# Optimization experiments

Measured on AMD Instinct MI355X. Metric: run time of the kernel, lower is better.

The kernel has to match this reference:

```python
import jax, jax.numpy as jnp
import numpy as np

SOBEL_X = jnp.array([[1., 0., -1.], [2., 0., -2.], [1., 0., -1.]], dtype=jnp.float32).reshape(1, 1, 3, 3)
SOBEL_Y = jnp.array([[1., 2., 1.], [0., 0., 0.], [-1., -2., -1.]], dtype=jnp.float32).reshape(1, 1, 3, 3)
EPS = 1e-3


def _sobel(img, kern):
    # img: [N, 1, H, W]; 3x3 conv, zero padding 1 (torch Conv2d padding=1)
    return jax.lax.conv_general_dilated(
        img, kern, window_strides=(1, 1), padding='SAME',
        dimension_numbers=('NCHW', 'OIHW', 'NCHW'))


def _compute_flow(frames):
    # frames: [B, T, 3, H, W] -> flow: [B, T-1, 2, H, W]
    B, T, C, H, W = frames.shape
    gray = (0.2989 * frames[:, :, 0] + 0.587 * frames[:, :, 1]
            + 0.114 * frames[:, :, 2])  # [B, T, H, W]
    I1 = gray[:, :-1].reshape(B * (T - 1), 1, H, W)
    I2 = gray[:, 1:].reshape(B * (T - 1), 1, H, W)
    Ix = _sobel(I1, SOBEL_X)
    Iy = _sobel(I1, SOBEL_Y)
    It = I2 - I1
    denom = Ix * Ix + Iy * Iy + EPS
    u = -Ix * It / denom
    v = -Iy * It / denom
    return jnp.concatenate([u, v], axis=1).reshape(B, T - 1, 2, H, W)


def setup_inputs() -> dict:
    key = jax.random.key(0)
    k1, k2 = jax.random.split(key)
    shape = (8, 8, 3, 256, 256)  # [B, T, C, H, W]
    pred = jax.random.uniform(k1, shape, dtype=jnp.float32)
    gt = jax.random.uniform(k2, shape, dtype=jnp.float32)
    return {"pred": pred, "gt": gt}


def reference(pred, gt):
    pred_flow = _compute_flow(pred)  # [B, T-1, 2, H, W]
    gt_flow = _compute_flow(gt)
    # motion magnitude: mean abs frame diff over channels, broadcast over 2 flow channels
    motion_mag = jnp.abs(gt[:, 1:] - gt[:, :-1]).mean(axis=2, keepdims=True)  # [B, T-1, 1, H, W]
    flow_loss = (jnp.abs(pred_flow - gt_flow) * motion_mag).mean()
    return flow_loss
```

## Files before the change

kernel.cpp:

```cpp
#include <hip/hip_runtime.h>

#define BB 8
#define TT 8
#define NPAIR (TT - 1)
#define HH 256
#define WW 256
#define FRAME_PIX (HH * WW)
#define RROWS 4
#define NSTRIP (HH / RROWS)
#define NITEM (BB * NPAIR * NSTRIP)
#define NBLK (NITEM / 4)
#define EPS 1e-3f
#define INV_N (1.0f / (float)((size_t)BB * NPAIR * 2 * HH * WW))

__device__ __forceinline__ float4 ld4(const float* __restrict__ p) {
    return *reinterpret_cast<const float4*>(p);
}
__device__ __forceinline__ float4 gray4(const float4 r, const float4 g, const float4 b) {
    float4 o;
    o.x = 0.2989f * r.x + 0.587f * g.x + 0.114f * b.x;
    o.y = 0.2989f * r.y + 0.587f * g.y + 0.114f * b.y;
    o.z = 0.2989f * r.z + 0.587f * g.z + 0.114f * b.z;
    o.w = 0.2989f * r.w + 0.587f * g.w + 0.114f * b.w;
    return o;
}

struct GRow { float l, a, b, c, d, r; };

__device__ __forceinline__ GRow mk_grow(const float4 g, const int lane) {
    GRow o;
    o.a = g.x; o.b = g.y; o.c = g.z; o.d = g.w;
    const float lw = __shfl_up(g.w, 1, 64);
    const float rx = __shfl_down(g.x, 1, 64);
    o.l = (lane == 0) ? 0.f : lw;
    o.r = (lane == 63) ? 0.f : rx;
    return o;
}

__device__ __forceinline__ void ld3(const float* __restrict__ base, const int y,
                                    const int X, float4& c0, float4& c1, float4& c2) {
    if ((unsigned)y < (unsigned)HH) {
        const float* q = base + (size_t)y * WW + X;
        c0 = ld4(q); c1 = ld4(q + FRAME_PIX); c2 = ld4(q + 2 * FRAME_PIX);
    } else {
        c0 = make_float4(0.f, 0.f, 0.f, 0.f); c1 = c0; c2 = c0;
    }
}

#define FLOWJ_P(T, M, Bt, f0, f1, f2, g2v, uj, vj)                              \
    {                                                                           \
        const float Ix = ((T).f0 - (T).f2) + 2.0f * ((M).f0 - (M).f2)           \
                       + ((Bt).f0 - (Bt).f2);                                   \
        const float Iy = ((T).f0 + 2.0f * (T).f1 + (T).f2)                      \
                       - ((Bt).f0 + 2.0f * (Bt).f1 + (Bt).f2);                  \
        const float It = (g2v) - (M).f1;                                        \
        const float inv = 1.0f / (Ix * Ix + Iy * Iy + EPS);                     \
        uj = -(Ix * It) * inv;                                                  \
        vj = -(Iy * It) * inv;                                                  \
    }

#define FLOWJ_G(T, M, Bt, f0, f1, f2, g2v, uj, vj, mmv)                         \
    {                                                                           \
        const float Ix = ((T).f0 - (T).f2) + 2.0f * ((M).f0 - (M).f2)           \
                       + ((Bt).f0 - (Bt).f2);                                   \
        const float Iy = ((T).f0 + 2.0f * (T).f1 + (T).f2)                      \
                       - ((Bt).f0 + 2.0f * (Bt).f1 + (Bt).f2);                  \
        const float It = (g2v) - (M).f1;                                        \
        const float inv = 1.0f / (Ix * Ix + Iy * Iy + EPS);                     \
        s += (fabsf((uj) + (Ix * It) * inv) + fabsf((vj) + (Iy * It) * inv))    \
             * (mmv);                                                           \
    }

#define STEP(ROWY)                                                              \
    {                                                                           \
        float4 pb0, pb1, pb2, gb0, gb1, gb2, pc0, pc1, pc2, gc0, gc1, gc2;      \
        ld3(p1, (ROWY) + 1, X, pb0, pb1, pb2);                                  \
        ld3(g1, (ROWY) + 1, X, gb0, gb1, gb2);                                  \
        ld3(p2, (ROWY), X, pc0, pc1, pc2);                                      \
        ld3(g2, (ROWY), X, gc0, gc1, gc2);                                      \
        const float mm0 = (fabsf(gc0.x - k0.x) + fabsf(gc1.x - k1.x)            \
                         + fabsf(gc2.x - k2.x)) * (1.f / 3.f);                  \
        const float mm1 = (fabsf(gc0.y - k0.y) + fabsf(gc1.y - k1.y)            \
                         + fabsf(gc2.y - k2.y)) * (1.f / 3.f);                  \
        const float mm2 = (fabsf(gc0.z - k0.z) + fabsf(gc1.z - k1.z)            \
                         + fabsf(gc2.z - k2.z)) * (1.f / 3.f);                  \
        const float mm3 = (fabsf(gc0.w - k0.w) + fabsf(gc1.w - k1.w)            \
                         + fabsf(gc2.w - k2.w)) * (1.f / 3.f);                  \
        const float4 gp2c = gray4(pc0, pc1, pc2);                               \
        const float4 gg2c = gray4(gc0, gc1, gc2);                               \
        const GRow pB = mk_grow(gray4(pb0, pb1, pb2), lane);                    \
        const GRow gB = mk_grow(gray4(gb0, gb1, gb2), lane);                    \
        k0 = gb0; k1 = gb1; k2 = gb2;                                           \
        float u0, u1, u2, u3, v0, v1, v2, v3;                                   \
        FLOWJ_P(pT, pM, pB, l, a, b, gp2c.x, u0, v0)                            \
        FLOWJ_P(pT, pM, pB, a, b, c, gp2c.y, u1, v1)                            \
        FLOWJ_P(pT, pM, pB, b, c, d, gp2c.z, u2, v2)                            \
        FLOWJ_P(pT, pM, pB, c, d, r, gp2c.w, u3, v3)                            \
        FLOWJ_G(gT, gM, gB, l, a, b, gg2c.x, u0, v0, mm0)                       \
        FLOWJ_G(gT, gM, gB, a, b, c, gg2c.y, u1, v1, mm1)                       \
        FLOWJ_G(gT, gM, gB, b, c, d, gg2c.z, u2, v2, mm2)                       \
        FLOWJ_G(gT, gM, gB, c, d, r, gg2c.w, u3, v3, mm3)                       \
        pT = pM; pM = pB;                                                       \
        gT = gM; gM = gB;                                                       \
    }

__global__ __launch_bounds__(256, 2) void flow_loss_kernel(
    const float* __restrict__ pred, const float* __restrict__ gt,
    float* __restrict__ partial)
{
    const int tid   = threadIdx.x;
    const int lane  = tid & 63;
    const int item  = blockIdx.x * 4 + (tid >> 6);
    const int strip = item & (NSTRIP - 1);
    const int pbt   = item >> 6;
    const int b     = pbt / NPAIR;
    const int t     = pbt - b * NPAIR;

    const size_t fs = (size_t)3 * FRAME_PIX;
    const float* p1 = pred + ((size_t)b * TT + t) * fs;
    const float* g1 = gt   + ((size_t)b * TT + t) * fs;
    const float* p2 = p1 + fs;
    const float* g2 = g1 + fs;

    const int X  = lane * 4;
    const int y0 = strip * RROWS;

    GRow pT, pM, gT, gM;
    float4 k0, k1, k2;

    {
        float4 a0, a1, a2, c0, c1, c2;
        ld3(p1, y0 - 1, X, a0, a1, a2);
        ld3(g1, y0 - 1, X, c0, c1, c2);
        pT = mk_grow(gray4(a0, a1, a2), lane);
        gT = mk_grow(gray4(c0, c1, c2), lane);
        ld3(p1, y0, X, a0, a1, a2);
        ld3(g1, y0, X, k0, k1, k2);
        pM = mk_grow(gray4(a0, a1, a2), lane);
        gM = mk_grow(gray4(k0, k1, k2), lane);
    }

    float s = 0.f;
    STEP(y0)
    STEP(y0 + 1)
    STEP(y0 + 2)
    STEP(y0 + 3)

    #pragma unroll
    for (int off = 32; off > 0; off >>= 1) s += __shfl_down(s, off, 64);
    if (lane == 0) partial[item] = s;
}

__global__ __launch_bounds__(896) void reduce_kernel(
    const float* __restrict__ partial, float* __restrict__ out)
{
    const float4 v = ld4(partial + threadIdx.x * 4);
    float s = (v.x + v.y) + (v.z + v.w);
    #pragma unroll
    for (int off = 32; off > 0; off >>= 1) s += __shfl_down(s, off, 64);

    __shared__ float wsum[14];
    if ((threadIdx.x & 63) == 0) wsum[threadIdx.x >> 6] = s;
    __syncthreads();
    if (threadIdx.x == 0) {
        float tot = 0.f;
        #pragma unroll
        for (int i = 0; i < 14; ++i) tot += wsum[i];
        out[0] = tot * INV_N;
    }
}

extern "C" void kernel_launch(void* const* d_in, const int* in_sizes, int n_in,
                              void* d_out, int out_size, void* d_ws, size_t ws_size,
                              hipStream_t stream) {
    const float* pred = (const float*)d_in[0];
    const float* gt   = (const float*)d_in[1];
    float* partial    = (float*)d_ws;
    float* out        = (float*)d_out;

    flow_loss_kernel<<<dim3(NBLK), dim3(256), 0, stream>>>(pred, gt, partial);
    reduce_kernel<<<1, 896, 0, stream>>>(partial, out);
}
```

Before: 124.1 us.

## Software-prefetch next frame-1 row and shrink blocks to two waves

Each step now issues the loads for the frame-1 row two ahead (y+2) while computing the current row, rotating the prefetched registers forward so global-load latency overlaps the Sobel/flow arithmetic. Blocks are reduced from 256 to 128 threads, with a launch bound of 3 blocks per CU and twice as many blocks in the grid. The prefetch raises register pressure, which may lower occupancy, and the memory-bound kernel may gain little since the total traffic is unchanged.

```diff
diff --git a/kernel.cpp b/kernel.cpp
--- a/kernel.cpp
+++ b/kernel.cpp
@@ -9,7 +9,7 @@
 #define RROWS 4
 #define NSTRIP (HH / RROWS)
 #define NITEM (BB * NPAIR * NSTRIP)
-#define NBLK (NITEM / 4)
+#define NBLK (NITEM / 2)
 #define EPS 1e-3f
 #define INV_N (1.0f / (float)((size_t)BB * NPAIR * 2 * HH * WW))
 
@@ -71,13 +71,21 @@
              * (mmv);                                                           \
     }
 
-#define STEP(ROWY)                                                              \
+#define STEP(ROWY, DO_PF)                                                       \
     {                                                                           \
-        float4 pb0, pb1, pb2, gb0, gb1, gb2, pc0, pc1, pc2, gc0, gc1, gc2;      \
-        ld3(p1, (ROWY) + 1, X, pb0, pb1, pb2);                                  \
-        ld3(g1, (ROWY) + 1, X, gb0, gb1, gb2);                                  \
+        float4 pc0, pc1, pc2, gc0, gc1, gc2;                                    \
         ld3(p2, (ROWY), X, pc0, pc1, pc2);                                      \
         ld3(g2, (ROWY), X, gc0, gc1, gc2);                                      \
+        float4 nbp0, nbp1, nbp2, nbg0, nbg1, nbg2;                              \
+        if (DO_PF) {                                                            \
+            ld3(p1, (ROWY) + 2, X, nbp0, nbp1, nbp2);                           \
+            ld3(g1, (ROWY) + 2, X, nbg0, nbg1, nbg2);                           \
+        } else {                                                                \
+            nbp0 = make_float4(0.f, 0.f, 0.f, 0.f); nbp1 = nbp0; nbp2 = nbp0;   \
+            nbg0 = nbp0; nbg1 = nbp0; nbg2 = nbp0;                              \
+        }                                                                       \
+        const GRow pB = mk_grow(gray4(fbp0, fbp1, fbp2), lane);                 \
+        const GRow gB = mk_grow(gray4(fbg0, fbg1, fbg2), lane);                 \
         const float mm0 = (fabsf(gc0.x - k0.x) + fabsf(gc1.x - k1.x)            \
                          + fabsf(gc2.x - k2.x)) * (1.f / 3.f);                  \
         const float mm1 = (fabsf(gc0.y - k0.y) + fabsf(gc1.y - k1.y)            \
@@ -88,9 +96,6 @@
                          + fabsf(gc2.w - k2.w)) * (1.f / 3.f);                  \
         const float4 gp2c = gray4(pc0, pc1, pc2);                               \
         const float4 gg2c = gray4(gc0, gc1, gc2);                               \
-        const GRow pB = mk_grow(gray4(pb0, pb1, pb2), lane);                    \
-        const GRow gB = mk_grow(gray4(gb0, gb1, gb2), lane);                    \
-        k0 = gb0; k1 = gb1; k2 = gb2;                                           \
         float u0, u1, u2, u3, v0, v1, v2, v3;                                   \
         FLOWJ_P(pT, pM, pB, l, a, b, gp2c.x, u0, v0)                            \
         FLOWJ_P(pT, pM, pB, a, b, c, gp2c.y, u1, v1)                            \
@@ -102,15 +107,18 @@
         FLOWJ_G(gT, gM, gB, c, d, r, gg2c.w, u3, v3, mm3)                       \
         pT = pM; pM = pB;                                                       \
         gT = gM; gM = gB;                                                       \
+        k0 = fbg0; k1 = fbg1; k2 = fbg2;                                        \
+        fbp0 = nbp0; fbp1 = nbp1; fbp2 = nbp2;                                  \
+        fbg0 = nbg0; fbg1 = nbg1; fbg2 = nbg2;                                  \
     }
 
-__global__ __launch_bounds__(256, 2) void flow_loss_kernel(
+__global__ __launch_bounds__(128, 3) void flow_loss_kernel(
     const float* __restrict__ pred, const float* __restrict__ gt,
     float* __restrict__ partial)
 {
     const int tid   = threadIdx.x;
     const int lane  = tid & 63;
-    const int item  = blockIdx.x * 4 + (tid >> 6);
+    const int item  = blockIdx.x * 2 + (tid >> 6);
     const int strip = item & (NSTRIP - 1);
     const int pbt   = item >> 6;
     const int b     = pbt / NPAIR;
@@ -127,24 +135,27 @@
 
     GRow pT, pM, gT, gM;
     float4 k0, k1, k2;
+    float4 fbp0, fbp1, fbp2, fbg0, fbg1, fbg2;
 
     {
         float4 a0, a1, a2, c0, c1, c2;
         ld3(p1, y0 - 1, X, a0, a1, a2);
         ld3(g1, y0 - 1, X, c0, c1, c2);
+        ld3(p1, y0, X, fbp0, fbp1, fbp2);
+        ld3(g1, y0, X, k0, k1, k2);
         pT = mk_grow(gray4(a0, a1, a2), lane);
         gT = mk_grow(gray4(c0, c1, c2), lane);
-        ld3(p1, y0, X, a0, a1, a2);
-        ld3(g1, y0, X, k0, k1, k2);
-        pM = mk_grow(gray4(a0, a1, a2), lane);
+        pM = mk_grow(gray4(fbp0, fbp1, fbp2), lane);
         gM = mk_grow(gray4(k0, k1, k2), lane);
+        ld3(p1, y0 + 1, X, fbp0, fbp1, fbp2);
+        ld3(g1, y0 + 1, X, fbg0, fbg1, fbg2);
     }
 
     float s = 0.f;
-    STEP(y0)
-    STEP(y0 + 1)
-    STEP(y0 + 2)
-    STEP(y0 + 3)
+    STEP(y0, 1)
+    STEP(y0 + 1, 1)
+    STEP(y0 + 2, 1)
+    STEP(y0 + 3, 0)
 
     #pragma unroll
     for (int off = 32; off > 0; off >>= 1) s += __shfl_down(s, off, 64);
@@ -178,6 +189,6 @@
     float* partial    = (float*)d_ws;
     float* out        = (float*)d_out;
 
-    flow_loss_kernel<<<dim3(NBLK), dim3(256), 0, stream>>>(pred, gt, partial);
+    flow_loss_kernel<<<dim3(NBLK), dim3(128), 0, stream>>>(pred, gt, partial);
     reduce_kernel<<<1, 896, 0, stream>>>(partial, out);
 }
```

After: 170.9 us. +37.7%, slower.
